# Kernel optimization log

Hardware: AMD Instinct MI355X
Metric: run time of the kernel (lower is better)

Reference implementation:

```python
import jax, jax.numpy as jnp
import numpy as np

N = 30000      # nodes
E = 400000     # edges per sparse set / GAT graph
F_IN = 512     # num_features
NHID = 128     # nhid
H = 4          # GAT heads
NCLS = 10      # num_classes
NSETS = 5      # num_gat = (3**2-1)//2 + 1
EPS = 1e-5     # BatchNorm eps


def setup_inputs() -> dict:
    key = jax.random.key(0)
    ks = jax.random.split(key, 24)
    s_in = 1.0 / np.sqrt(F_IN)
    s_h = 1.0 / np.sqrt(NHID)
    s_hh = 1.0 / np.sqrt(H * NHID)
    inp = {
        "x": jax.random.normal(ks[0], (N, F_IN), jnp.float32),
        "edge_index": jax.random.randint(ks[1], (2, E), 0, N),
        "scatter_idx": jax.random.randint(ks[2], (NSETS, 2, E), 0, N),
        "scatter_w": jax.random.normal(ks[3], (NSETS, E), jnp.float32) * 0.1,
        "lin_in_W": jax.random.normal(ks[4], (F_IN, NHID), jnp.float32) * s_in,
        "lin_in_b": jnp.zeros((NHID,), jnp.float32),
        "gat_W": jax.random.normal(ks[5], (NSETS, NHID, H * NHID), jnp.float32) * s_h,
        "att_src": jax.random.normal(ks[6], (NSETS, H, NHID), jnp.float32) * s_h,
        "att_dst": jax.random.normal(ks[7], (NSETS, H, NHID), jnp.float32) * s_h,
        "gat_b": jnp.zeros((NSETS, H * NHID), jnp.float32),
        "mlp_W": jax.random.normal(ks[8], (NSETS, H * NHID, NHID), jnp.float32) * s_hh,
        "mlp_b": jnp.zeros((NSETS, NHID), jnp.float32),
        "bn_g": jnp.ones((NSETS, NHID), jnp.float32),
        "bn_b": jnp.zeros((NSETS, NHID), jnp.float32),
        "bn_m": jax.random.normal(ks[9], (NSETS, NHID), jnp.float32) * 0.1,
        "bn_v": jax.random.uniform(ks[10], (NSETS, NHID), jnp.float32) + 0.5,
        "bn0_g": jnp.ones((NHID,), jnp.float32),
        "bn0_b": jnp.zeros((NHID,), jnp.float32),
        "bn0_m": jax.random.normal(ks[11], (NHID,), jnp.float32) * 0.1,
        "bn0_v": jax.random.uniform(ks[12], (NHID,), jnp.float32) + 0.5,
        "out_W": jax.random.normal(ks[13], (NHID, NCLS), jnp.float32) * s_h,
        "out_b": jnp.zeros((NCLS,), jnp.float32),
    }
    return inp


def _forward(x, edge_index, scatter_idx, scatter_w, lin_in_W, lin_in_b,
             gat_W, att_src, att_dst, gat_b, mlp_W, mlp_b,
             bn_g, bn_b, bn_m, bn_v, bn0_g, bn0_b, bn0_m, bn0_v, out_W, out_b):
    # solo_pass: gather source features, weight by edge value, scatter-add at dest
    def sp(i, xx):
        msg = scatter_w[i][:, None] * xx[scatter_idx[i, 0]]          # [E, NHID]
        return jax.ops.segment_sum(msg, scatter_idx[i, 1], num_segments=N)

    h = x @ lin_in_W + lin_in_b                                       # [N, NHID]
    x0 = sp(0, h)
    xhs = [jnp.abs(sp(i, h)) for i in range(1, NSETS)]
    xs = [x0] + [sp(0, xh) for xh in xhs]

    # GATConv adds self-loops by default
    loops = jnp.arange(N)
    src = jnp.concatenate([edge_index[0], loops])
    dst = jnp.concatenate([edge_index[1], loops])

    def gat(i, xx):
        hh = (xx @ gat_W[i]).reshape(N, H, NHID)                      # [N,H,C]
        a_s = (hh * att_src[i]).sum(-1)                               # [N,H]
        a_d = (hh * att_dst[i]).sum(-1)                               # [N,H]
        e = jax.nn.leaky_relu(a_s[src] + a_d[dst], 0.2)               # [E+N,H]
        m = jax.ops.segment_max(e, dst, num_segments=N)
        ex = jnp.exp(e - m[dst])
        den = jax.ops.segment_sum(ex, dst, num_segments=N)
        alpha = ex / (den[dst] + 1e-16)                               # [E+N,H]
        out = jax.ops.segment_sum(alpha[:, :, None] * hh[src], dst, num_segments=N)
        return out.reshape(N, H * NHID) + gat_b[i]

    # Seq(ELU, Dropout(eval=no-op), Linear, BatchNorm1d(eval))
    def mlp(i, xx):
        z = jax.nn.elu(xx) @ mlp_W[i] + mlp_b[i]
        return (z - bn_m[i]) * jax.lax.rsqrt(bn_v[i] + EPS) * bn_g[i] + bn_b[i]

    outs = [mlp(i, gat(i, xs[i])) for i in range(NSETS)]
    x_stage2 = h + outs[0] + outs[1] + outs[2] + outs[3] + outs[4]

    z = (x_stage2 - bn0_m) * jax.lax.rsqrt(bn0_v + EPS) * bn0_g + bn0_b
    z = jax.nn.elu(z) @ out_W + out_b
    return jax.nn.log_softmax(z, axis=1)


def reference(x, edge_index, scatter_idx, scatter_w, lin_in_W, lin_in_b,
              gat_W, att_src, att_dst, gat_b, mlp_W, mlp_b,
              bn_g, bn_b, bn_m, bn_v, bn0_g, bn0_b, bn0_m, bn0_v, out_W, out_b):
    return _forward(x, edge_index, scatter_idx, scatter_w, lin_in_W, lin_in_b,
                    gat_W, att_src, att_dst, gat_b, mlp_W, mlp_b,
                    bn_g, bn_b, bn_m, bn_v, bn0_g, bn0_b, bn0_m, bn0_v, out_W, out_b)
```

## Files before the change

kernel.cpp:

```cpp
#include <hip/hip_runtime.h>
#include <cstdint>
#include <cstddef>

#define NN 30000
#define NE 400000
#define EG (NE + NN)
#define NSETS 5
#define NCLS 10
#define BN_EPS 1e-5f

#define NBKT 118
#define CHUNK 4096
#define NWG_SET 98
#define NWG_GAT 105
#define NWGMAX 105
#define NBLK_BIN (5 * NWG_SET + NWG_GAT)
#define NBLK_SORT (6 * NBKT)

typedef __bf16 bf16x8 __attribute__((ext_vector_type(8)));
typedef float  f32x4  __attribute__((ext_vector_type(4)));

constexpr size_t alg(size_t x) { return (x + 255) & ~size_t(255); }
constexpr size_t OFF_U1    = 0;
constexpr size_t OFF_HB    = OFF_U1   + alg((size_t)5 * NN * 128 * 2);
// ... 118 lines not shown
    __shared__ int s[128];
    int tot = 0;
    if (t < NBKT) {
        const int* p = bh + (size_t)(g * NBKT + t) * NWGMAX;
        for (int w = 0; w < nwg; ++w) tot += p[w];
    }
    s[t] = tot;
    __syncthreads();
    for (int d = 1; d < 128; d <<= 1) {
        int u = (t >= d) ? s[t - d] : 0;
        __syncthreads();
        s[t] += u;
        __syncthreads();
    }
    if (t < NBKT) bb[g * 132 + t] = s[t] - tot;
    if (t == NBKT - 1) {
        bb[g * 132 + NBKT] = s[t];
        off6[g * (NN + 1) + NN] = s[t];
    }
}

__global__ void wgscan(const int* __restrict__ bb, int* __restrict__ bh) {
    const int gb = blockIdx.x;
    const int g = gb / NBKT, bk = gb - g * NBKT;
    __shared__ int s[128];
    const int t = threadIdx.x;
    const int nwg = (g < 5) ? NWG_SET : NWG_GAT;
    int v = (t < nwg) ? bh[(size_t)gb * NWGMAX + t] : 0;
    s[t] = v;
    __syncthreads();
    for (int d = 1; d < 128; d <<= 1) {
        int u = (t >= d) ? s[t - d] : 0;
        __syncthreads();
        s[t] += u;
        __syncthreads();
    }
    const int base = bb[g * 132 + bk];
    if (t < nwg) bh[(size_t)gb * NWGMAX + t] = base + (s[t] - v);
}

__global__ void __launch_bounds__(256) binP(const int* __restrict__ scat_idx, const float* __restrict__ scat_w,
                                            const int* __restrict__ edge_ix, const int* __restrict__ pos,
                                            int2* __restrict__ stg_sp, int* __restrict__ stg_g) {
    __shared__ int lpos[NBKT];
    __shared__ int lcur[NBKT];
    int g, wg, e0, e1;
    chunk_map(blockIdx.x, g, wg, e0, e1);
    for (int i = threadIdx.x; i < NBKT; i += 256) {
        lpos[i] = pos[(size_t)(g * NBKT + i) * NWGMAX + wg];
        lcur[i] = 0;
    }
    __syncthreads();
    if (g < 5) {
        const int* si = scat_idx + (size_t)g * 2 * NE;
        const float* sw = scat_w + (size_t)g * NE;
        for (int e = e0 + threadIdx.x; e < e1; e += 256) {
            int src = si[e], d = si[NE + e];
            int r = atomicAdd(&lcur[d >> 8], 1);
            int2 pk; pk.x = src | (d << 15); pk.y = __float_as_int(sw[e]);
            stg_sp[(size_t)g * NE + lpos[d >> 8] + r] = pk;
        }
    } else {
        for (int e = e0 + threadIdx.x; e < e1; e += 256) {
            int src, d;
            if (e < NE) { src = edge_ix[e]; d = edge_ix[NE + e]; }
            else        { src = e - NE;     d = src; }
            int r = atomicAdd(&lcur[d >> 8], 1);
            stg_g[lpos[d >> 8] + r] = src | (d << 15);
        }
    }
}

__global__ void __launch_bounds__(256) sortP(const int* __restrict__ bb,
                                             const int2* __restrict__ stg_sp, const int* __restrict__ stg_g,
                                             int2* __restrict__ spp, int* __restrict__ g_src,
                                             int* __restrict__ off6) {
    __shared__ int lcnt[256];
    __shared__ int loff[257];
    const int gb = blockIdx.x;
    const int g = gb / NBKT, bk = gb - g * NBKT;
    const int n0 = bk << 8;
    const int nlen = min(256, NN - n0);
    const int base = bb[g * 132 + bk];
    const int end  = bb[g * 132 + bk + 1];
    const int t = threadIdx.x;
    lcnt[t] = 0;
    __syncthreads();
    if (g < 5) {
        for (int j = base + t; j < end; j += 256)
            atomicAdd(&lcnt[((stg_sp[(size_t)g * NE + j].x >> 15) & 0x7fff) - n0], 1);
    } else {
        for (int j = base + t; j < end; j += 256)
            atomicAdd(&lcnt[((stg_g[j] >> 15) & 0x7fff) - n0], 1);
    }
    __syncthreads();
    int v = lcnt[t];
    __syncthreads();
    for (int d = 1; d < 256; d <<= 1) {
        int u = (t >= d) ? lcnt[t - d] : 0;
        __syncthreads();
        lcnt[t] += u;
        __syncthreads();
    }
    loff[t] = base + lcnt[t] - v;
    if (t == 255) loff[256] = base + lcnt[255];
    __syncthreads();
    if (t < nlen) off6[g * (NN + 1) + n0 + t] = loff[t];
    lcnt[t] = 0;
    __syncthreads();
    if (g < 5) {
        for (int j = base + t; j < end; j += 256) {
            int2 pk = stg_sp[(size_t)g * NE + j];
            int ln = ((pk.x >> 15) & 0x7fff) - n0;
            int p = loff[ln] + atomicAdd(&lcnt[ln], 1);
            int2 o; o.x = pk.x & 0x7fff; o.y = pk.y;
            spp[(size_t)g * NE + p] = o;
        }
    } else {
        for (int j = base + t; j < end; j += 256) {
            int w = stg_g[j];
            int ln = ((w >> 15) & 0x7fff) - n0;
            int p = loff[ln] + atomicAdd(&lcnt[ln], 1);
            g_src[p] = w & 0x7fff;
        }
    }
}

template<int ROWS>
__device__ __forceinline__ void stage64(const unsigned short* __restrict__ src, int ld,
                                        int row0, int maxrow, int k0, char* lds, int t) {
    const int wave = t >> 6, lane = t & 63;
    const int sub = lane >> 3;
    const int kch = (lane & 7) ^ sub;
    for (int j = wave; j < ROWS / 8; j += 4) {
        int grow = row0 + j * 8 + sub;
        if (grow > maxrow) grow = maxrow;
        gload_lds16(src + (size_t)grow * ld + k0 + kch * 8, lds + j * 1024);
    }
}

__global__ void __launch_bounds__(256) mgemm_lin(const unsigned short* __restrict__ A,
                                                 const unsigned short* __restrict__ BT,
                                                 const float* __restrict__ bias,
                                                 unsigned short* __restrict__ outb,
                                                 float* __restrict__ x2) {
    constexpr int K = 512, NC = 128;
    __shared__ __align__(16) char As[64 * 128];
    __shared__ __align__(16) char Bs[128 * 128];
    const int t = threadIdx.x, wave = t >> 6, lane = t & 63;
    const int bm = blockIdx.x * 64;
    const int wr = (wave >> 1) * 32, wc = (wave & 1) * 64;
    const int l15 = lane & 15, l4 = lane >> 4;
    const int rsw = (l15 & 7) << 4;
    f32x4 acc[2][4] = {};

    for (int kt = 0; kt < K; kt += 64) {
        stage64<64>(A, K, bm, NN - 1, kt, As, t);
        stage64<128>(BT, K, 0, NC - 1, kt, Bs, t);
        __syncthreads();
        #pragma unroll
        for (int kk = 0; kk < 2; ++kk) {
            bf16x8 af[2], bf[4];
            const int koff = kk * 64 + l4 * 16;
            #pragma unroll
            for (int fm = 0; fm < 2; ++fm)
                af[fm] = *(const bf16x8*)(As + (wr + fm * 16 + l15) * 128 + (koff ^ rsw));
            #pragma unroll
            for (int fn = 0; fn < 4; ++fn)
                bf[fn] = *(const bf16x8*)(Bs + (wc + fn * 16 + l15) * 128 + (koff ^ rsw));
            #pragma unroll
            for (int fm = 0; fm < 2; ++fm)
                #pragma unroll
                for (int fn = 0; fn < 4; ++fn)
                    acc[fm][fn] = __builtin_amdgcn_mfma_f32_16x16x32_bf16(af[fm], bf[fn], acc[fm][fn], 0, 0, 0);
        }
        __syncthreads();
    }

    #pragma unroll
    for (int fn = 0; fn < 4; ++fn) {
        const int c = wc + fn * 16 + l15;
        const float bias_c = bias[c];
        #pragma unroll
        for (int fm = 0; fm < 2; ++fm) {
            #pragma unroll
            for (int rg = 0; rg < 4; ++rg) {
                int r = bm + wr + fm * 16 + l4 * 4 + rg;
                if (r < NN) {
                    float v = acc[fm][fn][rg] + bias_c;
                    outb[(size_t)r * NC + c] = f2bf(v);
                    x2[(size_t)r * NC + c] = v;
                }
            }
        }
    }
}

__global__ void __launch_bounds__(256) fusedGM(const unsigned short* __restrict__ agg,
                                               const unsigned short* __restrict__ gatWT,
                                               const unsigned short* __restrict__ mlpWT,
                                               const float* __restrict__ gat_b,
                                               const float* __restrict__ mlp_b,
                                               const float* __restrict__ bng, const float* __restrict__ bnb,
                                               const float* __restrict__ bnm, const float* __restrict__ bnv,
                                               float* __restrict__ x2) {
    __shared__ __align__(16) char U[49152];
    __shared__ __align__(16) char gtile[16384];
    const int t = threadIdx.x, wave = t >> 6, lane = t & 63;
    const int bm = blockIdx.x * 64;
    const int wr = (wave >> 1) * 32, wc = (wave & 1) * 64;
    const int l15 = lane & 15, l4 = lane >> 4;
    const int rsw = (l15 & 7) << 4;
    f32x4 acc2[2][4] = {};

    #pragma unroll
    for (int h = 0; h < 4; ++h) {
        stage64<64>(agg, 512, bm, NN - 1, h * 128,       U,         t);
        stage64<64>(agg, 512, bm, NN - 1, h * 128 + 64,  U + 8192,  t);
        stage64<128>(gatWT, 128, h * 128, 511, 0,        U + 16384, t);
        stage64<128>(gatWT, 128, h * 128, 511, 64,       U + 32768, t);
        __syncthreads();

        f32x4 a1[2][4] = {};
        #pragma unroll
        for (int ks = 0; ks < 4; ++ks) {
            const char* Asb = U + (ks >> 1) * 8192;
            const char* Bsb = U + 16384 + (ks >> 1) * 16384;
            const int koff = (ks & 1) * 64 + l4 * 16;
            bf16x8 af[2], bf[4];
            #pragma unroll
            for (int fm = 0; fm < 2; ++fm)
                af[fm] = *(const bf16x8*)(Asb + (wr + fm * 16 + l15) * 128 + (koff ^ rsw));
            #pragma unroll
            for (int fn = 0; fn < 4; ++fn)
                bf[fn] = *(const bf16x8*)(Bsb + (wc + fn * 16 + l15) * 128 + (koff ^ rsw));
            #pragma unroll
            for (int fm = 0; fm < 2; ++fm)
                #pragma unroll
                for (int fn = 0; fn < 4; ++fn)
                    a1[fm][fn] = __builtin_amdgcn_mfma_f32_16x16x32_bf16(af[fm], bf[fn], a1[fm][fn], 0, 0, 0);
        }
        __syncthreads();

        #pragma unroll
        for (int fn = 0; fn < 4; ++fn) {
            const int cc = wc + fn * 16 + l15;
            const float gb = gat_b[h * 128 + cc];
            #pragma unroll
            for (int fm = 0; fm < 2; ++fm) {
                #pragma unroll
                for (int rg = 0; rg < 4; ++rg) {
                    const int r = wr + fm * 16 + l4 * 4 + rg;
                    const unsigned short v = f2bf(eluf(a1[fm][fn][rg] + gb));
                    *(unsigned short*)(gtile + r * 256 + ((((cc >> 3) ^ (r & 7)) << 4) | ((cc & 7) << 1))) = v;
                }
            }
        }
        stage64<128>(mlpWT, 512, 0, 127, h * 128,      U,         t);
        stage64<128>(mlpWT, 512, 0, 127, h * 128 + 64, U + 16384, t);
        __syncthreads();

        #pragma unroll
        for (int ks = 0; ks < 4; ++ks) {
            const int s2 = ks >> 1, kk = ks & 1;
            const char* slab = U + s2 * 16384;
            bf16x8 af[2], bf[4];
            #pragma unroll
            for (int fm = 0; fm < 2; ++fm) {
                const int r2 = wr + fm * 16 + l15;
                const int chunk = (s2 * 8 + kk * 4 + l4) ^ (r2 & 7);
                af[fm] = *(const bf16x8*)(gtile + r2 * 256 + (chunk << 4));
            }
            const int koff = kk * 64 + l4 * 16;
            #pragma unroll
            for (int fn = 0; fn < 4; ++fn)
                bf[fn] = *(const bf16x8*)(slab + (wc + fn * 16 + l15) * 128 + (koff ^ rsw));
            #pragma unroll
            for (int fm = 0; fm < 2; ++fm)
                #pragma unroll
                for (int fn = 0; fn < 4; ++fn)
                    acc2[fm][fn] = __builtin_amdgcn_mfma_f32_16x16x32_bf16(af[fm], bf[fn], acc2[fm][fn], 0, 0, 0);
        }
        __syncthreads();
    }

    #pragma unroll
    for (int fn = 0; fn < 4; ++fn) {
        const int c = wc + fn * 16 + l15;
        const float sc = bng[c] * rsqrtf(bnv[c] + BN_EPS);
        const float sh = bnb[c] - bnm[c] * sc;
        const float mb = mlp_b[c];
        #pragma unroll
        for (int fm = 0; fm < 2; ++fm) {
            #pragma unroll
            for (int rg = 0; rg < 4; ++rg) {
                int r = bm + wr + fm * 16 + l4 * 4 + rg;
                if (r < NN)
                    x2[(size_t)r * 128 + c] += (acc2[fm][fn][rg] + mb) * sc + sh;
            }
        }
    }
}

__global__ void __launch_bounds__(256) sp_abs4(const int* __restrict__ off6,
                                               const int2* __restrict__ spp,
                                               const unsigned short* __restrict__ hb,
                                               unsigned short* __restrict__ tmp4) {
    const int y = blockIdx.y;
    const int* off = off6 + (y + 1) * (NN + 1);
    const int2* pk = spp + (size_t)(y + 1) * NE;
    unsigned short* out = tmp4 + (size_t)y * NN * 128;

    const int wid  = blockIdx.x * 4 + (threadIdx.x >> 6);
    const int lane = threadIdx.x & 63;
    const int co   = lane * 2;
    const int s0 = off[wid], s1 = off[wid + 1];
    float a0 = 0.f, a1 = 0.f;
    int j = s0;
    for (; j + 7 < s1; j += 8) {
        int2 e[8];
        unsigned v[8];
        #pragma unroll
        for (int q = 0; q < 8; ++q) e[q] = pk[j + q];
        #pragma unroll
        for (int q = 0; q < 8; ++q) v[q] = *(const unsigned*)(hb + (size_t)e[q].x * 128 + co);
        #pragma unroll
        for (int q = 0; q < 8; ++q) {
            float w = __int_as_float(e[q].y);
            a0 = fmaf(w, bf2f(v[q] & 0xffffu), a0);
            a1 = fmaf(w, bf2f(v[q] >> 16), a1);
        }
    }
    for (; j < s1; ++j) {
        int2 e = pk[j];
        float wj = __int_as_float(e.y);
        unsigned v = *(const unsigned*)(hb + (size_t)e.x * 128 + co);
        a0 = fmaf(wj, bf2f(v & 0xffffu), a0);
        a1 = fmaf(wj, bf2f(v >> 16), a1);
    }
    a0 = fabsf(a0); a1 = fabsf(a1);
    unsigned o = (unsigned)f2bf(a0) | ((unsigned)f2bf(a1) << 16);
    *(unsigned*)(out + (size_t)wid * 128 + co) = o;
}

__global__ void __launch_bounds__(256) sp_fused5(const int* __restrict__ off0,
                                                 const int2* __restrict__ spp0,
                                                 const unsigned short* __restrict__ hb,
                                                 const unsigned short* __restrict__ tmp4,
                                                 unsigned short* __restrict__ xcur5,
                                                 const float* __restrict__ watt,
                                                 float* __restrict__ as5,
                                                 float* __restrict__ ad5) {
    __shared__ float sWatt[5120];
    for (int i = threadIdx.x; i < 5120; i += 256) sWatt[i] = watt[i];
    __syncthreads();

    const int wid  = blockIdx.x * 4 + (threadIdx.x >> 6);
    const int lane = threadIdx.x & 63;
    const int co   = lane * 2;
    const int s0 = off0[wid], s1 = off0[wid + 1];
    const unsigned short* t0 = tmp4;
    const unsigned short* t1 = tmp4 + (size_t)1 * NN * 128;
    const unsigned short* t2 = tmp4 + (size_t)2 * NN * 128;
    const unsigned short* t3 = tmp4 + (size_t)3 * NN * 128;

    float a[5][2] = {};
    int j = s0;
    for (; j + 1 < s1; j += 2) {
        int2 eA = spp0[j], eB = spp0[j + 1];
        size_t rA = (size_t)eA.x * 128 + co, rB = (size_t)eB.x * 128 + co;
        unsigned vA0 = *(const unsigned*)(hb + rA), vB0 = *(const unsigned*)(hb + rB);
        unsigned vA1 = *(const unsigned*)(t0 + rA), vB1 = *(const unsigned*)(t0 + rB);
        unsigned vA2 = *(const unsigned*)(t1 + rA), vB2 = *(const unsigned*)(t1 + rB);
        unsigned vA3 = *(const unsigned*)(t2 + rA), vB3 = *(const unsigned*)(t2 + rB);
        unsigned vA4 = *(const unsigned*)(t3 + rA), vB4 = *(const unsigned*)(t3 + rB);
        float wA = __int_as_float(eA.y), wB = __int_as_float(eB.y);
        a[0][0] = fmaf(wA, bf2f(vA0 & 0xffffu), a[0][0]); a[0][1] = fmaf(wA, bf2f(vA0 >> 16), a[0][1]);
        a[1][0] = fmaf(wA, bf2f(vA1 & 0xffffu), a[1][0]); a[1][1] = fmaf(wA, bf2f(vA1 >> 16), a[1][1]);
        a[2][0] = fmaf(wA, bf2f(vA2 & 0xffffu), a[2][0]); a[2][1] = fmaf(wA, bf2f(vA2 >> 16), a[2][1]);
        a[3][0] = fmaf(wA, bf2f(vA3 & 0xffffu), a[3][0]); a[3][1] = fmaf(wA, bf2f(vA3 >> 16), a[3][1]);
        a[4][0] = fmaf(wA, bf2f(vA4 & 0xffffu), a[4][0]); a[4][1] = fmaf(wA, bf2f(vA4 >> 16), a[4][1]);
        a[0][0] = fmaf(wB, bf2f(vB0 & 0xffffu), a[0][0]); a[0][1] = fmaf(wB, bf2f(vB0 >> 16), a[0][1]);
        a[1][0] = fmaf(wB, bf2f(vB1 & 0xffffu), a[1][0]); a[1][1] = fmaf(wB, bf2f(vB1 >> 16), a[1][1]);
        a[2][0] = fmaf(wB, bf2f(vB2 & 0xffffu), a[2][0]); a[2][1] = fmaf(wB, bf2f(vB2 >> 16), a[2][1]);
        a[3][0] = fmaf(wB, bf2f(vB3 & 0xffffu), a[3][0]); a[3][1] = fmaf(wB, bf2f(vB3 >> 16), a[3][1]);
        a[4][0] = fmaf(wB, bf2f(vB4 & 0xffffu), a[4][0]); a[4][1] = fmaf(wB, bf2f(vB4 >> 16), a[4][1]);
    }
    if (j < s1) {
        int2 e = spp0[j];
        size_t r = (size_t)e.x * 128 + co;
        unsigned v0 = *(const unsigned*)(hb + r);
        unsigned v1 = *(const unsigned*)(t0 + r);
        unsigned v2 = *(const unsigned*)(t1 + r);
        unsigned v3 = *(const unsigned*)(t2 + r);
        unsigned v4 = *(const unsigned*)(t3 + r);
        float wj = __int_as_float(e.y);
        a[0][0] = fmaf(wj, bf2f(v0 & 0xffffu), a[0][0]); a[0][1] = fmaf(wj, bf2f(v0 >> 16), a[0][1]);
        a[1][0] = fmaf(wj, bf2f(v1 & 0xffffu), a[1][0]); a[1][1] = fmaf(wj, bf2f(v1 >> 16), a[1][1]);
        a[2][0] = fmaf(wj, bf2f(v2 & 0xffffu), a[2][0]); a[2][1] = fmaf(wj, bf2f(v2 >> 16), a[2][1]);
        a[3][0] = fmaf(wj, bf2f(v3 & 0xffffu), a[3][0]); a[3][1] = fmaf(wj, bf2f(v3 >> 16), a[3][1]);
        a[4][0] = fmaf(wj, bf2f(v4 & 0xffffu), a[4][0]); a[4][1] = fmaf(wj, bf2f(v4 >> 16), a[4][1]);
    }
    #pragma unroll
    for (int y = 0; y < 5; ++y) {
        unsigned o = (unsigned)f2bf(a[y][0]) | ((unsigned)f2bf(a[y][1]) << 16);
        *(unsigned*)(xcur5 + (size_t)y * NN * 128 + (size_t)wid * 128 + co) = o;
    }

    #pragma unroll
    for (int i = 0; i < 5; ++i) {
        #pragma unroll
        for (int h = 0; h < 4; ++h) {
            const float* wS = sWatt + ((i * 2 + 0) * 4 + h) * 128;
            const float* wD = sWatt + ((i * 2 + 1) * 4 + h) * 128;
            float ps = a[i][0] * wS[co] + a[i][1] * wS[co + 1];
            float pd = a[i][0] * wD[co] + a[i][1] * wD[co + 1];
            #pragma unroll
            for (int dd = 1; dd < 64; dd <<= 1) { ps += __shfl_xor(ps, dd); pd += __shfl_xor(pd, dd); }
            if (lane == 0) {
                as5[(size_t)i * NN * 4 + (size_t)wid * 4 + h] = ps;
                ad5[(size_t)i * NN * 4 + (size_t)wid * 4 + h] = pd;
            }
        }
    }
}

__device__ __forceinline__ void acc8(float* a, float al, uint4 v) {
    a[0] = fmaf(al, bf2f(v.x & 0xffffu), a[0]); a[1] = fmaf(al, bf2f(v.x >> 16), a[1]);
    a[2] = fmaf(al, bf2f(v.y & 0xffffu), a[2]); a[3] = fmaf(al, bf2f(v.y >> 16), a[3]);
    a[4] = fmaf(al, bf2f(v.z & 0xffffu), a[4]); a[5] = fmaf(al, bf2f(v.z >> 16), a[5]);
    a[6] = fmaf(al, bf2f(v.w & 0xffffu), a[6]); a[7] = fmaf(al, bf2f(v.w >> 16), a[7]);
}

__global__ void __launch_bounds__(256) gat_agg2(const int* __restrict__ goff, const int* __restrict__ gsrc,
                                                const float* __restrict__ as_, const float* __restrict__ ad_,
                                                const unsigned short* __restrict__ xcur,
                                                unsigned short* __restrict__ agg) {
    const int wid  = blockIdx.x * 4 + (threadIdx.x >> 6);
    const int lane = threadIdx.x & 63;
    const int hd   = lane >> 4;
    const int cl   = (lane & 15) * 8;
    const int s0 = goff[wid], s1 = goff[wid + 1];
    const float4 adv4 = *(const float4*)(ad_ + (size_t)wid * 4);

    float m[4] = {-1e30f, -1e30f, -1e30f, -1e30f};
    float s[4] = {0.f, 0.f, 0.f, 0.f};
    for (int j = s0 + lane; j < s1; j += 64) {
        const int si = gsrc[j];
        float4 av = *(const float4*)(as_ + (size_t)si * 4);
        float e[4] = {lrelu02(av.x + adv4.x), lrelu02(av.y + adv4.y),
                      lrelu02(av.z + adv4.z), lrelu02(av.w + adv4.w)};
        #pragma unroll
        for (int h = 0; h < 4; ++h) {
            if (e[h] > m[h]) { s[h] = s[h] * __expf(m[h] - e[h]) + 1.f; m[h] = e[h]; }
            else             { s[h] += __expf(e[h] - m[h]); }
        }
    }
    #pragma unroll
    for (int d = 1; d < 64; d <<= 1) {
        #pragma unroll
        for (int h = 0; h < 4; ++h) {
            float om = __shfl_xor(m[h], d);
            float os = __shfl_xor(s[h], d);
            float nm = fmaxf(m[h], om);
            s[h] = s[h] * __expf(m[h] - nm) + os * __expf(om - nm);
            m[h] = nm;
        }
    }
    const float advh = hd == 0 ? adv4.x : hd == 1 ? adv4.y : hd == 2 ? adv4.z : adv4.w;
    const float mv   = hd == 0 ? m[0]   : hd == 1 ? m[1]   : hd == 2 ? m[2]   : m[3];
    const float dv   = hd == 0 ? s[0]   : hd == 1 ? s[1]   : hd == 2 ? s[2]   : s[3];
    const float inv  = 1.f / (dv + 1e-16f);

    float ac[8] = {};
    int j = s0;
    for (; j + 3 < s1; j += 4) {
        int i0 = gsrc[j], i1 = gsrc[j + 1], i2 = gsrc[j + 2], i3 = gsrc[j + 3];
        float q0 = as_[(size_t)i0 * 4 + hd], q1 = as_[(size_t)i1 * 4 + hd];
        float q2 = as_[(size_t)i2 * 4 + hd], q3 = as_[(size_t)i3 * 4 + hd];
        uint4 v0 = *(const uint4*)(xcur + (size_t)i0 * 128 + cl);
        uint4 v1 = *(const uint4*)(xcur + (size_t)i1 * 128 + cl);
        uint4 v2 = *(const uint4*)(xcur + (size_t)i2 * 128 + cl);
        uint4 v3 = *(const uint4*)(xcur + (size_t)i3 * 128 + cl);
        float al0 = __expf(lrelu02(q0 + advh) - mv) * inv;
        float al1 = __expf(lrelu02(q1 + advh) - mv) * inv;
        float al2 = __expf(lrelu02(q2 + advh) - mv) * inv;
        float al3 = __expf(lrelu02(q3 + advh) - mv) * inv;
        acc8(ac, al0, v0); acc8(ac, al1, v1); acc8(ac, al2, v2); acc8(ac, al3, v3);
    }
    for (; j < s1; ++j) {
        int si = gsrc[j];
        float q = as_[(size_t)si * 4 + hd];
        uint4 v = *(const uint4*)(xcur + (size_t)si * 128 + cl);
        float al = __expf(lrelu02(q + advh) - mv) * inv;
        acc8(ac, al, v);
    }
    uint4 ov;
    ov.x = (unsigned)f2bf(ac[0]) | ((unsigned)f2bf(ac[1]) << 16);
    ov.y = (unsigned)f2bf(ac[2]) | ((unsigned)f2bf(ac[3]) << 16);
    ov.z = (unsigned)f2bf(ac[4]) | ((unsigned)f2bf(ac[5]) << 16);
    ov.w = (unsigned)f2bf(ac[6]) | ((unsigned)f2bf(ac[7]) << 16);
    *(uint4*)(agg + (size_t)wid * 512 + hd * 128 + cl) = ov;
}

__global__ void __launch_bounds__(256) final_out(const float* __restrict__ x2,
                                                 const float* __restrict__ bn0g, const float* __restrict__ bn0b,
                                                 const float* __restrict__ bn0m, const float* __restrict__ bn0v,
                                                 const float* __restrict__ outW, const float* __restrict__ outb,
                                                 float* __restrict__ out) {
    __shared__ float sW[128 * 12];
    __shared__ float sSc[128], sSh[128];
    for (int i = threadIdx.x; i < 1280; i += 256) {
        int r = i / 10, c = i - r * 10;
        sW[r * 12 + c] = outW[i];
    }
    if (threadIdx.x < 128) {
        int c = threadIdx.x;
        float sc = bn0g[c] * rsqrtf(bn0v[c] + BN_EPS);
        sSc[c] = sc;
        sSh[c] = bn0b[c] - bn0m[c] * sc;
    }
    __syncthreads();
    const int wid  = blockIdx.x * 4 + (threadIdx.x >> 6);
    const int lane = threadIdx.x & 63;
    const int c0 = lane * 2;
    float2 a = *(const float2*)(x2 + (size_t)wid * 128 + c0);
    float a0 = eluf(a.x * sSc[c0] + sSh[c0]);
    float a1 = eluf(a.y * sSc[c0 + 1] + sSh[c0 + 1]);
    float p[NCLS];
    #pragma unroll
    for (int j = 0; j < NCLS; ++j)
        p[j] = a0 * sW[c0 * 12 + j] + a1 * sW[(c0 + 1) * 12 + j];
    #pragma unroll
    for (int j = 0; j < NCLS; ++j) {
        float v = p[j];
        v += __shfl_xor(v, 1);  v += __shfl_xor(v, 2);  v += __shfl_xor(v, 4);
        v += __shfl_xor(v, 8);  v += __shfl_xor(v, 16); v += __shfl_xor(v, 32);
        p[j] = v;
    }
    float z[NCLS];
    #pragma unroll
    for (int j = 0; j < NCLS; ++j) z[j] = p[j] + outb[j];
    float m = z[0];
    #pragma unroll
    for (int j = 1; j < NCLS; ++j) m = fmaxf(m, z[j]);
    float ssum = 0.f;
    #pragma unroll
    for (int j = 0; j < NCLS; ++j) ssum += __expf(z[j] - m);
    float lse = m + __logf(ssum);
    #pragma unroll
    for (int j = 0; j < NCLS; ++j)
        if (lane == j) out[(size_t)wid * NCLS + j] = z[j] - lse;
}

extern "C" void kernel_launch(void* const* d_in, const int* in_sizes, int n_in,
                              void* d_out, int out_size, void* d_ws, size_t ws_size,
                              hipStream_t stream) {
    const float* x        = (const float*)d_in[0];
    const int*   edge_ix  = (const int*)  d_in[1];
    const int*   scat_idx = (const int*)  d_in[2];
    const float* scat_w   = (const float*)d_in[3];
    const float* lin_W    = (const float*)d_in[4];
    const float* lin_b    = (const float*)d_in[5];
    const float* gat_W    = (const float*)d_in[6];
    const float* att_src  = (const float*)d_in[7];
    const float* att_dst  = (const float*)d_in[8];
    const float* gat_b    = (const float*)d_in[9];
    const float* mlp_W    = (const float*)d_in[10];
    const float* mlp_b    = (const float*)d_in[11];
    const float* bn_g     = (const float*)d_in[12];
    const float* bn_b     = (const float*)d_in[13];
    const float* bn_m     = (const float*)d_in[14];
    const float* bn_v     = (const float*)d_in[15];
    const float* bn0_g    = (const float*)d_in[16];
    const float* bn0_b    = (const float*)d_in[17];
    const float* bn0_m    = (const float*)d_in[18];
    const float* bn0_v    = (const float*)d_in[19];
    const float* out_W    = (const float*)d_in[20];
    const float* out_b    = (const float*)d_in[21];
    float* out = (float*)d_out;

    char* ws = (char*)d_ws;
    unsigned short* xb    = (unsigned short*)(ws + OFF_U1);
    unsigned short* xcur5 = (unsigned short*)(ws + OFF_U1);
    unsigned short* hb    = (unsigned short*)(ws + OFF_HB);
    float*          x2    = (float*)(ws + OFF_X2);
    unsigned short* agg   = (unsigned short*)(ws + OFF_AGG);
    unsigned short* tmp4  = (unsigned short*)(ws + OFF_GOUT);
    int2*  stg_sp = (int2*)(ws + OFF_GOUT);
    int*   stg_g  = (int*)(ws + OFF_GOUT + (size_t)NSETS * NE * 8);
    unsigned short* wt    = (unsigned short*)(ws + OFF_WT);
    unsigned short* linWT = wt;
    unsigned short* gatWT = wt + 65536;
    unsigned short* mlpWT = wt + 65536 * 6;
    float* watt   = (float*)(ws + OFF_WATT);
    int*   off6   = (int*)(ws + OFF_OFF6);
    int2*  spp    = (int2*)(ws + OFF_SPP);
    int*   g_src  = (int*)(ws + OFF_GSRC);
    int*   bh     = (int*)(ws + OFF_CNT);
    int*   bb     = bh + NBLK_SORT * NWGMAX;
    float* as5    = (float*)(ws + OFF_AS5);
    float* ad5    = (float*)(ws + OFF_AD5);

    const dim3 b256(256);

    prep1<<<PREP_GRID, b256, 0, stream>>>(scat_idx, edge_ix, bh, x, xb,
                                          lin_W, gat_W, mlp_W, linWT, gatWT, mlpWT,
                                          att_src, att_dst, watt);
    bktscan<<<6, 128, 0, stream>>>(bh, bb, off6);
    wgscan<<<NBLK_SORT, 128, 0, stream>>>(bb, bh);
    binP<<<NBLK_BIN, b256, 0, stream>>>(scat_idx, scat_w, edge_ix, bh, stg_sp, stg_g);
    sortP<<<NBLK_SORT, b256, 0, stream>>>(bb, stg_sp, stg_g, spp, g_src, off6);

    mgemm_lin<<<469, b256, 0, stream>>>(xb, linWT, lin_b, hb, x2);

    sp_abs4<<<dim3(7500, 4), b256, 0, stream>>>(off6, spp, hb, tmp4);
    sp_fused5<<<7500, b256, 0, stream>>>(off6, spp, hb, tmp4, xcur5, watt, as5, ad5);

    for (int i = 0; i < NSETS; ++i) {
        gat_agg2<<<7500, b256, 0, stream>>>(off6 + 5 * (NN + 1), g_src,
                                            as5 + (size_t)i * NN * 4, ad5 + (size_t)i * NN * 4,
                                            xcur5 + (size_t)i * NN * 128, agg);
        fusedGM<<<469, b256, 0, stream>>>(agg, gatWT + (size_t)i * 65536, mlpWT + (size_t)i * 65536,
                                          gat_b + (size_t)i * 512, mlp_b + (size_t)i * 128,
                                          bn_g + (size_t)i * 128, bn_b + (size_t)i * 128,
                                          bn_m + (size_t)i * 128, bn_v + (size_t)i * 128, x2);
    }

    final_out<<<7500, b256, 0, stream>>>(x2, bn0_g, bn0_b, bn0_m, bn0_v, out_W, out_b, out);
}
```

Measured before the change: 680.4 us.

## Split GAT aggregation edges across lane groups, compute all heads per group

```diff
diff --git a/kernel.cpp b/kernel.cpp
--- a/kernel.cpp
+++ b/kernel.cpp
@@ -501,47 +501,43 @@
     const int lane = threadIdx.x & 63;
     const int co   = lane * 2;
     const int s0 = off0[wid], s1 = off0[wid + 1];
-    const unsigned short* t0 = tmp4;
-    const unsigned short* t1 = tmp4 + (size_t)1 * NN * 128;
-    const unsigned short* t2 = tmp4 + (size_t)2 * NN * 128;
-    const unsigned short* t3 = tmp4 + (size_t)3 * NN * 128;
+    const unsigned short* tbl[5] = {
+        hb, tmp4, tmp4 + (size_t)1 * NN * 128, tmp4 + (size_t)2 * NN * 128, tmp4 + (size_t)3 * NN * 128 };
 
     float a[5][2] = {};
     int j = s0;
-    for (; j + 1 < s1; j += 2) {
-        int2 eA = spp0[j], eB = spp0[j + 1];
-        size_t rA = (size_t)eA.x * 128 + co, rB = (size_t)eB.x * 128 + co;
-        unsigned vA0 = *(const unsigned*)(hb + rA), vB0 = *(const unsigned*)(hb + rB);
-        unsigned vA1 = *(const unsigned*)(t0 + rA), vB1 = *(const unsigned*)(t0 + rB);
-        unsigned vA2 = *(const unsigned*)(t1 + rA), vB2 = *(const unsigned*)(t1 + rB);
-        unsigned vA3 = *(const unsigned*)(t2 + rA), vB3 = *(const unsigned*)(t2 + rB);
-        unsigned vA4 = *(const unsigned*)(t3 + rA), vB4 = *(const unsigned*)(t3 + rB);
-        float wA = __int_as_float(eA.y), wB = __int_as_float(eB.y);
-        a[0][0] = fmaf(wA, bf2f(vA0 & 0xffffu), a[0][0]); a[0][1] = fmaf(wA, bf2f(vA0 >> 16), a[0][1]);
-        a[1][0] = fmaf(wA, bf2f(vA1 & 0xffffu), a[1][0]); a[1][1] = fmaf(wA, bf2f(vA1 >> 16), a[1][1]);
-        a[2][0] = fmaf(wA, bf2f(vA2 & 0xffffu), a[2][0]); a[2][1] = fmaf(wA, bf2f(vA2 >> 16), a[2][1]);
-        a[3][0] = fmaf(wA, bf2f(vA3 & 0xffffu), a[3][0]); a[3][1] = fmaf(wA, bf2f(vA3 >> 16), a[3][1]);
-        a[4][0] = fmaf(wA, bf2f(vA4 & 0xffffu), a[4][0]); a[4][1] = fmaf(wA, bf2f(vA4 >> 16), a[4][1]);
-        a[0][0] = fmaf(wB, bf2f(vB0 & 0xffffu), a[0][0]); a[0][1] = fmaf(wB, bf2f(vB0 >> 16), a[0][1]);
-        a[1][0] = fmaf(wB, bf2f(vB1 & 0xffffu), a[1][0]); a[1][1] = fmaf(wB, bf2f(vB1 >> 16), a[1][1]);
-        a[2][0] = fmaf(wB, bf2f(vB2 & 0xffffu), a[2][0]); a[2][1] = fmaf(wB, bf2f(vB2 >> 16), a[2][1]);
-        a[3][0] = fmaf(wB, bf2f(vB3 & 0xffffu), a[3][0]); a[3][1] = fmaf(wB, bf2f(vB3 >> 16), a[3][1]);
-        a[4][0] = fmaf(wB, bf2f(vB4 & 0xffffu), a[4][0]); a[4][1] = fmaf(wB, bf2f(vB4 >> 16), a[4][1]);
-    }
-    if (j < s1) {
+    for (; j + 3 < s1; j += 4) {
+        int2 e0 = spp0[j], e1 = spp0[j + 1], e2 = spp0[j + 2], e3 = spp0[j + 3];
+        size_t r0 = (size_t)e0.x * 128 + co, r1 = (size_t)e1.x * 128 + co;
+        size_t r2 = (size_t)e2.x * 128 + co, r3 = (size_t)e3.x * 128 + co;
+        unsigned v[5][4];
+        #pragma unroll
+        for (int y = 0; y < 5; ++y) {
+            v[y][0] = *(const unsigned*)(tbl[y] + r0);
+            v[y][1] = *(const unsigned*)(tbl[y] + r1);
+            v[y][2] = *(const unsigned*)(tbl[y] + r2);
+            v[y][3] = *(const unsigned*)(tbl[y] + r3);
+        }
+        float w0 = __int_as_float(e0.y), w1 = __int_as_float(e1.y);
+        float w2 = __int_as_float(e2.y), w3 = __int_as_float(e3.y);
+        #pragma unroll
+        for (int y = 0; y < 5; ++y) {
+            a[y][0] = fmaf(w0, bf2f(v[y][0] & 0xffffu), a[y][0]); a[y][1] = fmaf(w0, bf2f(v[y][0] >> 16), a[y][1]);
+            a[y][0] = fmaf(w1, bf2f(v[y][1] & 0xffffu), a[y][0]); a[y][1] = fmaf(w1, bf2f(v[y][1] >> 16), a[y][1]);
+            a[y][0] = fmaf(w2, bf2f(v[y][2] & 0xffffu), a[y][0]); a[y][1] = fmaf(w2, bf2f(v[y][2] >> 16), a[y][1]);
+            a[y][0] = fmaf(w3, bf2f(v[y][3] & 0xffffu), a[y][0]); a[y][1] = fmaf(w3, bf2f(v[y][3] >> 16), a[y][1]);
+        }
+    }
+    for (; j < s1; ++j) {
         int2 e = spp0[j];
         size_t r = (size_t)e.x * 128 + co;
-        unsigned v0 = *(const unsigned*)(hb + r);
-        unsigned v1 = *(const unsigned*)(t0 + r);
-        unsigned v2 = *(const unsigned*)(t1 + r);
-        unsigned v3 = *(const unsigned*)(t2 + r);
-        unsigned v4 = *(const unsigned*)(t3 + r);
         float wj = __int_as_float(e.y);
-        a[0][0] = fmaf(wj, bf2f(v0 & 0xffffu), a[0][0]); a[0][1] = fmaf(wj, bf2f(v0 >> 16), a[0][1]);
-        a[1][0] = fmaf(wj, bf2f(v1 & 0xffffu), a[1][0]); a[1][1] = fmaf(wj, bf2f(v1 >> 16), a[1][1]);
-        a[2][0] = fmaf(wj, bf2f(v2 & 0xffffu), a[2][0]); a[2][1] = fmaf(wj, bf2f(v2 >> 16), a[2][1]);
-        a[3][0] = fmaf(wj, bf2f(v3 & 0xffffu), a[3][0]); a[3][1] = fmaf(wj, bf2f(v3 >> 16), a[3][1]);
-        a[4][0] = fmaf(wj, bf2f(v4 & 0xffffu), a[4][0]); a[4][1] = fmaf(wj, bf2f(v4 >> 16), a[4][1]);
+        #pragma unroll
+        for (int y = 0; y < 5; ++y) {
+            unsigned v = *(const unsigned*)(tbl[y] + r);
+            a[y][0] = fmaf(wj, bf2f(v & 0xffffu), a[y][0]);
+            a[y][1] = fmaf(wj, bf2f(v >> 16), a[y][1]);
+        }
     }
     #pragma unroll
     for (int y = 0; y < 5; ++y) {
@@ -567,21 +563,15 @@
     }
 }
 
-__device__ __forceinline__ void acc8(float* a, float al, uint4 v) {
-    a[0] = fmaf(al, bf2f(v.x & 0xffffu), a[0]); a[1] = fmaf(al, bf2f(v.x >> 16), a[1]);
-    a[2] = fmaf(al, bf2f(v.y & 0xffffu), a[2]); a[3] = fmaf(al, bf2f(v.y >> 16), a[3]);
-    a[4] = fmaf(al, bf2f(v.z & 0xffffu), a[4]); a[5] = fmaf(al, bf2f(v.z >> 16), a[5]);
-    a[6] = fmaf(al, bf2f(v.w & 0xffffu), a[6]); a[7] = fmaf(al, bf2f(v.w >> 16), a[7]);
-}
-
-__global__ void __launch_bounds__(256) gat_agg2(const int* __restrict__ goff, const int* __restrict__ gsrc,
+__global__ void __launch_bounds__(256) gat_agg3(const int* __restrict__ goff, const int* __restrict__ gsrc,
                                                 const float* __restrict__ as_, const float* __restrict__ ad_,
                                                 const unsigned short* __restrict__ xcur,
                                                 unsigned short* __restrict__ agg) {
     const int wid  = blockIdx.x * 4 + (threadIdx.x >> 6);
     const int lane = threadIdx.x & 63;
-    const int hd   = lane >> 4;
-    const int cl   = (lane & 15) * 8;
+    const int g    = lane >> 4;
+    const int p    = lane & 15;
+    const int cl   = p * 8;
     const int s0 = goff[wid], s1 = goff[wid + 1];
     const float4 adv4 = *(const float4*)(ad_ + (size_t)wid * 4);
 
@@ -609,40 +599,72 @@
             m[h] = nm;
         }
     }
-    const float advh = hd == 0 ? adv4.x : hd == 1 ? adv4.y : hd == 2 ? adv4.z : adv4.w;
-    const float mv   = hd == 0 ? m[0]   : hd == 1 ? m[1]   : hd == 2 ? m[2]   : m[3];
-    const float dv   = hd == 0 ? s[0]   : hd == 1 ? s[1]   : hd == 2 ? s[2]   : s[3];
-    const float inv  = 1.f / (dv + 1e-16f);
-
-    float ac[8] = {};
-    int j = s0;
-    for (; j + 3 < s1; j += 4) {
-        int i0 = gsrc[j], i1 = gsrc[j + 1], i2 = gsrc[j + 2], i3 = gsrc[j + 3];
-        float q0 = as_[(size_t)i0 * 4 + hd], q1 = as_[(size_t)i1 * 4 + hd];
-        float q2 = as_[(size_t)i2 * 4 + hd], q3 = as_[(size_t)i3 * 4 + hd];
-        uint4 v0 = *(const uint4*)(xcur + (size_t)i0 * 128 + cl);
-        uint4 v1 = *(const uint4*)(xcur + (size_t)i1 * 128 + cl);
-        uint4 v2 = *(const uint4*)(xcur + (size_t)i2 * 128 + cl);
-        uint4 v3 = *(const uint4*)(xcur + (size_t)i3 * 128 + cl);
-        float al0 = __expf(lrelu02(q0 + advh) - mv) * inv;
-        float al1 = __expf(lrelu02(q1 + advh) - mv) * inv;
-        float al2 = __expf(lrelu02(q2 + advh) - mv) * inv;
-        float al3 = __expf(lrelu02(q3 + advh) - mv) * inv;
-        acc8(ac, al0, v0); acc8(ac, al1, v1); acc8(ac, al2, v2); acc8(ac, al3, v3);
-    }
-    for (; j < s1; ++j) {
-        int si = gsrc[j];
-        float q = as_[(size_t)si * 4 + hd];
+    float mv[4], inv[4];
+    #pragma unroll
+    for (int h = 0; h < 4; ++h) { mv[h] = m[h]; inv[h] = 1.f / (s[h] + 1e-16f); }
+
+    float ac[4][8] = {};
+    int j = s0 + g;
+    for (; j + 4 < s1; j += 8) {
+        const int iA = gsrc[j], iB = gsrc[j + 4];
+        float4 avA = *(const float4*)(as_ + (size_t)iA * 4);
+        float4 avB = *(const float4*)(as_ + (size_t)iB * 4);
+        uint4 vA = *(const uint4*)(xcur + (size_t)iA * 128 + cl);
+        uint4 vB = *(const uint4*)(xcur + (size_t)iB * 128 + cl);
+        float alA[4], alB[4];
+        #pragma unroll
+        for (int h = 0; h < 4; ++h) {
+            alA[h] = __expf(lrelu02((&avA.x)[h] + (&adv4.x)[h]) - mv[h]) * inv[h];
+            alB[h] = __expf(lrelu02((&avB.x)[h] + (&adv4.x)[h]) - mv[h]) * inv[h];
+        }
+        const unsigned* wA = (const unsigned*)&vA;
+        const unsigned* wB = (const unsigned*)&vB;
+        #pragma unroll
+        for (int c = 0; c < 4; ++c) {
+            float lA = bf2f(wA[c] & 0xffffu), hA = bf2f(wA[c] >> 16);
+            float lB = bf2f(wB[c] & 0xffffu), hB = bf2f(wB[c] >> 16);
+            #pragma unroll
+            for (int h = 0; h < 4; ++h) {
+                ac[h][c * 2]     = fmaf(alA[h], lA, ac[h][c * 2]);
+                ac[h][c * 2 + 1] = fmaf(alA[h], hA, ac[h][c * 2 + 1]);
+                ac[h][c * 2]     = fmaf(alB[h], lB, ac[h][c * 2]);
+                ac[h][c * 2 + 1] = fmaf(alB[h], hB, ac[h][c * 2 + 1]);
+            }
+        }
+    }
+    for (; j < s1; j += 4) {
+        const int si = gsrc[j];
+        float4 av = *(const float4*)(as_ + (size_t)si * 4);
         uint4 v = *(const uint4*)(xcur + (size_t)si * 128 + cl);
-        float al = __expf(lrelu02(q + advh) - mv) * inv;
-        acc8(ac, al, v);
-    }
+        float al[4];
+        #pragma unroll
+        for (int h = 0; h < 4; ++h)
+            al[h] = __expf(lrelu02((&av.x)[h] + (&adv4.x)[h]) - mv[h]) * inv[h];
+        const unsigned* w = (const unsigned*)&v;
+        #pragma unroll
+        for (int c = 0; c < 4; ++c) {
+            float lo = bf2f(w[c] & 0xffffu), hi = bf2f(w[c] >> 16);
+            #pragma unroll
+            for (int h = 0; h < 4; ++h) {
+                ac[h][c * 2]     = fmaf(al[h], lo, ac[h][c * 2]);
+                ac[h][c * 2 + 1] = fmaf(al[h], hi, ac[h][c * 2 + 1]);
+            }
+        }
+    }
+    #pragma unroll
+    for (int d = 16; d < 64; d <<= 1)
+        #pragma unroll
+        for (int h = 0; h < 4; ++h)
+            #pragma unroll
+            for (int c = 0; c < 8; ++c)
+                ac[h][c] += __shfl_xor(ac[h][c], d);
+
     uint4 ov;
-    ov.x = (unsigned)f2bf(ac[0]) | ((unsigned)f2bf(ac[1]) << 16);
-    ov.y = (unsigned)f2bf(ac[2]) | ((unsigned)f2bf(ac[3]) << 16);
-    ov.z = (unsigned)f2bf(ac[4]) | ((unsigned)f2bf(ac[5]) << 16);
-    ov.w = (unsigned)f2bf(ac[6]) | ((unsigned)f2bf(ac[7]) << 16);
-    *(uint4*)(agg + (size_t)wid * 512 + hd * 128 + cl) = ov;
+    ov.x = (unsigned)f2bf(ac[g][0]) | ((unsigned)f2bf(ac[g][1]) << 16);
+    ov.y = (unsigned)f2bf(ac[g][2]) | ((unsigned)f2bf(ac[g][3]) << 16);
+    ov.z = (unsigned)f2bf(ac[g][4]) | ((unsigned)f2bf(ac[g][5]) << 16);
+    ov.w = (unsigned)f2bf(ac[g][6]) | ((unsigned)f2bf(ac[g][7]) << 16);
+    *(uint4*)(agg + (size_t)wid * 512 + g * 128 + cl) = ov;
 }
 
 __global__ void __launch_bounds__(256) final_out(const float* __restrict__ x2,
@@ -760,7 +782,7 @@
     sp_fused5<<<7500, b256, 0, stream>>>(off6, spp, hb, tmp4, xcur5, watt, as5, ad5);
 
     for (int i = 0; i < NSETS; ++i) {
-        gat_agg2<<<7500, b256, 0, stream>>>(off6 + 5 * (NN + 1), g_src,
+        gat_agg3<<<7500, b256, 0, stream>>>(off6 + 5 * (NN + 1), g_src,
                                             as5 + (size_t)i * NN * 4, ad5 + (size_t)i * NN * 4,
                                             xcur5 + (size_t)i * NN * 128, agg);
         fusedGM<<<469, b256, 0, stream>>>(agg, gatWT + (size_t)i * 65536, mlpWT + (size_t)i * 65536,
```

New measurement: 785.9 us. +15.5%, slower.

## Interleave four abs-scatter outputs per node for single vector gather

Applied to the files above, without the earlier changes.

```diff
diff --git a/kernel.cpp b/kernel.cpp
--- a/kernel.cpp
+++ b/kernel.cpp
@@ -444,51 +444,56 @@
     }
 }
 
-__global__ void __launch_bounds__(256) sp_abs4(const int* __restrict__ off6,
-                                               const int2* __restrict__ spp,
-                                               const unsigned short* __restrict__ hb,
-                                               unsigned short* __restrict__ tmp4) {
-    const int y = blockIdx.y;
-    const int* off = off6 + (y + 1) * (NN + 1);
-    const int2* pk = spp + (size_t)(y + 1) * NE;
-    unsigned short* out = tmp4 + (size_t)y * NN * 128;
-
+__global__ void __launch_bounds__(256) sp_abs_all(const int* __restrict__ off6,
+                                                  const int2* __restrict__ spp,
+                                                  const unsigned short* __restrict__ hb,
+                                                  unsigned short* __restrict__ tmpI) {
     const int wid  = blockIdx.x * 4 + (threadIdx.x >> 6);
     const int lane = threadIdx.x & 63;
     const int co   = lane * 2;
-    const int s0 = off[wid], s1 = off[wid + 1];
-    float a0 = 0.f, a1 = 0.f;
-    int j = s0;
-    for (; j + 7 < s1; j += 8) {
-        int2 e[8];
-        unsigned v[8];
-        #pragma unroll
-        for (int q = 0; q < 8; ++q) e[q] = pk[j + q];
-        #pragma unroll
-        for (int q = 0; q < 8; ++q) v[q] = *(const unsigned*)(hb + (size_t)e[q].x * 128 + co);
-        #pragma unroll
-        for (int q = 0; q < 8; ++q) {
-            float w = __int_as_float(e[q].y);
-            a0 = fmaf(w, bf2f(v[q] & 0xffffu), a0);
-            a1 = fmaf(w, bf2f(v[q] >> 16), a1);
-        }
-    }
-    for (; j < s1; ++j) {
-        int2 e = pk[j];
-        float wj = __int_as_float(e.y);
-        unsigned v = *(const unsigned*)(hb + (size_t)e.x * 128 + co);
-        a0 = fmaf(wj, bf2f(v & 0xffffu), a0);
-        a1 = fmaf(wj, bf2f(v >> 16), a1);
-    }
-    a0 = fabsf(a0); a1 = fabsf(a1);
-    unsigned o = (unsigned)f2bf(a0) | ((unsigned)f2bf(a1) << 16);
-    *(unsigned*)(out + (size_t)wid * 128 + co) = o;
+    float a[4][2];
+    #pragma unroll
+    for (int y = 0; y < 4; ++y) {
+        const int* off = off6 + (y + 1) * (NN + 1);
+        const int2* pk = spp + (size_t)(y + 1) * NE;
+        const int s0 = off[wid], s1 = off[wid + 1];
+        float a0 = 0.f, a1 = 0.f;
+        int j = s0;
+        for (; j + 3 < s1; j += 4) {
+            int2 e0 = pk[j], e1 = pk[j + 1], e2 = pk[j + 2], e3 = pk[j + 3];
+            unsigned v0 = *(const unsigned*)(hb + (size_t)e0.x * 128 + co);
+            unsigned v1 = *(const unsigned*)(hb + (size_t)e1.x * 128 + co);
+            unsigned v2 = *(const unsigned*)(hb + (size_t)e2.x * 128 + co);
+            unsigned v3 = *(const unsigned*)(hb + (size_t)e3.x * 128 + co);
+            float w0 = __int_as_float(e0.y), w1 = __int_as_float(e1.y);
+            float w2 = __int_as_float(e2.y), w3 = __int_as_float(e3.y);
+            a0 = fmaf(w0, bf2f(v0 & 0xffffu), a0); a1 = fmaf(w0, bf2f(v0 >> 16), a1);
+            a0 = fmaf(w1, bf2f(v1 & 0xffffu), a0); a1 = fmaf(w1, bf2f(v1 >> 16), a1);
+            a0 = fmaf(w2, bf2f(v2 & 0xffffu), a0); a1 = fmaf(w2, bf2f(v2 >> 16), a1);
+            a0 = fmaf(w3, bf2f(v3 & 0xffffu), a0); a1 = fmaf(w3, bf2f(v3 >> 16), a1);
+        }
+        for (; j < s1; ++j) {
+            int2 e = pk[j];
+            float wj = __int_as_float(e.y);
+            unsigned v = *(const unsigned*)(hb + (size_t)e.x * 128 + co);
+            a0 = fmaf(wj, bf2f(v & 0xffffu), a0);
+            a1 = fmaf(wj, bf2f(v >> 16), a1);
+        }
+        a[y][0] = fabsf(a0);
+        a[y][1] = fabsf(a1);
+    }
+    uint4 o;
+    o.x = (unsigned)f2bf(a[0][0]) | ((unsigned)f2bf(a[1][0]) << 16);
+    o.y = (unsigned)f2bf(a[2][0]) | ((unsigned)f2bf(a[3][0]) << 16);
+    o.z = (unsigned)f2bf(a[0][1]) | ((unsigned)f2bf(a[1][1]) << 16);
+    o.w = (unsigned)f2bf(a[2][1]) | ((unsigned)f2bf(a[3][1]) << 16);
+    *(uint4*)(tmpI + (size_t)wid * 512 + co * 4) = o;
 }
 
 __global__ void __launch_bounds__(256) sp_fused5(const int* __restrict__ off0,
                                                  const int2* __restrict__ spp0,
                                                  const unsigned short* __restrict__ hb,
-                                                 const unsigned short* __restrict__ tmp4,
+                                                 const unsigned short* __restrict__ tmpI,
                                                  unsigned short* __restrict__ xcur5,
                                                  const float* __restrict__ watt,
                                                  float* __restrict__ as5,
@@ -501,48 +506,40 @@
     const int lane = threadIdx.x & 63;
     const int co   = lane * 2;
     const int s0 = off0[wid], s1 = off0[wid + 1];
-    const unsigned short* t0 = tmp4;
-    const unsigned short* t1 = tmp4 + (size_t)1 * NN * 128;
-    const unsigned short* t2 = tmp4 + (size_t)2 * NN * 128;
-    const unsigned short* t3 = tmp4 + (size_t)3 * NN * 128;
 
     float a[5][2] = {};
     int j = s0;
-    for (; j + 1 < s1; j += 2) {
-        int2 eA = spp0[j], eB = spp0[j + 1];
-        size_t rA = (size_t)eA.x * 128 + co, rB = (size_t)eB.x * 128 + co;
-        unsigned vA0 = *(const unsigned*)(hb + rA), vB0 = *(const unsigned*)(hb + rB);
-        unsigned vA1 = *(const unsigned*)(t0 + rA), vB1 = *(const unsigned*)(t0 + rB);
-        unsigned vA2 = *(const unsigned*)(t1 + rA), vB2 = *(const unsigned*)(t1 + rB);
-        unsigned vA3 = *(const unsigned*)(t2 + rA), vB3 = *(const unsigned*)(t2 + rB);
-        unsigned vA4 = *(const unsigned*)(t3 + rA), vB4 = *(const unsigned*)(t3 + rB);
-        float wA = __int_as_float(eA.y), wB = __int_as_float(eB.y);
-        a[0][0] = fmaf(wA, bf2f(vA0 & 0xffffu), a[0][0]); a[0][1] = fmaf(wA, bf2f(vA0 >> 16), a[0][1]);
-        a[1][0] = fmaf(wA, bf2f(vA1 & 0xffffu), a[1][0]); a[1][1] = fmaf(wA, bf2f(vA1 >> 16), a[1][1]);
-        a[2][0] = fmaf(wA, bf2f(vA2 & 0xffffu), a[2][0]); a[2][1] = fmaf(wA, bf2f(vA2 >> 16), a[2][1]);
-        a[3][0] = fmaf(wA, bf2f(vA3 & 0xffffu), a[3][0]); a[3][1] = fmaf(wA, bf2f(vA3 >> 16), a[3][1]);
-        a[4][0] = fmaf(wA, bf2f(vA4 & 0xffffu), a[4][0]); a[4][1] = fmaf(wA, bf2f(vA4 >> 16), a[4][1]);
-        a[0][0] = fmaf(wB, bf2f(vB0 & 0xffffu), a[0][0]); a[0][1] = fmaf(wB, bf2f(vB0 >> 16), a[0][1]);
-        a[1][0] = fmaf(wB, bf2f(vB1 & 0xffffu), a[1][0]); a[1][1] = fmaf(wB, bf2f(vB1 >> 16), a[1][1]);
-        a[2][0] = fmaf(wB, bf2f(vB2 & 0xffffu), a[2][0]); a[2][1] = fmaf(wB, bf2f(vB2 >> 16), a[2][1]);
-        a[3][0] = fmaf(wB, bf2f(vB3 & 0xffffu), a[3][0]); a[3][1] = fmaf(wB, bf2f(vB3 >> 16), a[3][1]);
-        a[4][0] = fmaf(wB, bf2f(vB4 & 0xffffu), a[4][0]); a[4][1] = fmaf(wB, bf2f(vB4 >> 16), a[4][1]);
-    }
-    if (j < s1) {
+    for (; j + 3 < s1; j += 4) {
+        int2 e0 = spp0[j], e1 = spp0[j + 1], e2 = spp0[j + 2], e3 = spp0[j + 3];
+        unsigned h0 = *(const unsigned*)(hb + (size_t)e0.x * 128 + co);
+        unsigned h1 = *(const unsigned*)(hb + (size_t)e1.x * 128 + co);
+        unsigned h2 = *(const unsigned*)(hb + (size_t)e2.x * 128 + co);
+        unsigned h3 = *(const unsigned*)(hb + (size_t)e3.x * 128 + co);
+        uint4 t0 = *(const uint4*)(tmpI + (size_t)e0.x * 512 + co * 4);
+        uint4 t1 = *(const uint4*)(tmpI + (size_t)e1.x * 512 + co * 4);
+        uint4 t2 = *(const uint4*)(tmpI + (size_t)e2.x * 512 + co * 4);
+        uint4 t3 = *(const uint4*)(tmpI + (size_t)e3.x * 512 + co * 4);
+        float w0 = __int_as_float(e0.y), w1 = __int_as_float(e1.y);
+        float w2 = __int_as_float(e2.y), w3 = __int_as_float(e3.y);
+        #define ACC1(W, H, T) \
+            a[0][0] = fmaf(W, bf2f((H) & 0xffffu), a[0][0]); a[0][1] = fmaf(W, bf2f((H) >> 16), a[0][1]); \
+            a[1][0] = fmaf(W, bf2f((T).x & 0xffffu), a[1][0]); a[2][0] = fmaf(W, bf2f((T).x >> 16), a[2][0]); \
+            a[3][0] = fmaf(W, bf2f((T).y & 0xffffu), a[3][0]); a[4][0] = fmaf(W, bf2f((T).y >> 16), a[4][0]); \
+            a[1][1] = fmaf(W, bf2f((T).z & 0xffffu), a[1][1]); a[2][1] = fmaf(W, bf2f((T).z >> 16), a[2][1]); \
+            a[3][1] = fmaf(W, bf2f((T).w & 0xffffu), a[3][1]); a[4][1] = fmaf(W, bf2f((T).w >> 16), a[4][1]);
+        ACC1(w0, h0, t0)
+        ACC1(w1, h1, t1)
+        ACC1(w2, h2, t2)
+        ACC1(w3, h3, t3)
+    }
+    for (; j < s1; ++j) {
         int2 e = spp0[j];
-        size_t r = (size_t)e.x * 128 + co;
-        unsigned v0 = *(const unsigned*)(hb + r);
-        unsigned v1 = *(const unsigned*)(t0 + r);
-        unsigned v2 = *(const unsigned*)(t1 + r);
-        unsigned v3 = *(const unsigned*)(t2 + r);
-        unsigned v4 = *(const unsigned*)(t3 + r);
         float wj = __int_as_float(e.y);
-        a[0][0] = fmaf(wj, bf2f(v0 & 0xffffu), a[0][0]); a[0][1] = fmaf(wj, bf2f(v0 >> 16), a[0][1]);
-        a[1][0] = fmaf(wj, bf2f(v1 & 0xffffu), a[1][0]); a[1][1] = fmaf(wj, bf2f(v1 >> 16), a[1][1]);
-        a[2][0] = fmaf(wj, bf2f(v2 & 0xffffu), a[2][0]); a[2][1] = fmaf(wj, bf2f(v2 >> 16), a[2][1]);
-        a[3][0] = fmaf(wj, bf2f(v3 & 0xffffu), a[3][0]); a[3][1] = fmaf(wj, bf2f(v3 >> 16), a[3][1]);
-        a[4][0] = fmaf(wj, bf2f(v4 & 0xffffu), a[4][0]); a[4][1] = fmaf(wj, bf2f(v4 >> 16), a[4][1]);
-    }
+        unsigned hh = *(const unsigned*)(hb + (size_t)e.x * 128 + co);
+        uint4 tt = *(const uint4*)(tmpI + (size_t)e.x * 512 + co * 4);
+        ACC1(wj, hh, tt)
+    }
+    #undef ACC1
     #pragma unroll
     for (int y = 0; y < 5; ++y) {
         unsigned o = (unsigned)f2bf(a[y][0]) | ((unsigned)f2bf(a[y][1]) << 16);
@@ -728,7 +725,7 @@
     unsigned short* hb    = (unsigned short*)(ws + OFF_HB);
     float*          x2    = (float*)(ws + OFF_X2);
     unsigned short* agg   = (unsigned short*)(ws + OFF_AGG);
-    unsigned short* tmp4  = (unsigned short*)(ws + OFF_GOUT);
+    unsigned short* tmpI  = (unsigned short*)(ws + OFF_GOUT);
     int2*  stg_sp = (int2*)(ws + OFF_GOUT);
     int*   stg_g  = (int*)(ws + OFF_GOUT + (size_t)NSETS * NE * 8);
     unsigned short* wt    = (unsigned short*)(ws + OFF_WT);
@@ -756,8 +753,8 @@
 
     mgemm_lin<<<469, b256, 0, stream>>>(xb, linWT, lin_b, hb, x2);
 
-    sp_abs4<<<dim3(7500, 4), b256, 0, stream>>>(off6, spp, hb, tmp4);
-    sp_fused5<<<7500, b256, 0, stream>>>(off6, spp, hb, tmp4, xcur5, watt, as5, ad5);
+    sp_abs_all<<<7500, b256, 0, stream>>>(off6, spp, hb, tmpI);
+    sp_fused5<<<7500, b256, 0, stream>>>(off6, spp, hb, tmpI, xcur5, watt, as5, ad5);
 
     for (int i = 0; i < NSETS; ++i) {
         gat_agg2<<<7500, b256, 0, stream>>>(off6 + 5 * (NN + 1), g_src,
```

New measurement: 679.4 us. About the same (-0.1%).
